# Kernel optimization log

Measured on AMD Instinct MI355X. Metric: run time of the kernel, lower is better.

The kernel has to match this reference:

```python
import jax, jax.numpy as jnp
import numpy as np

SR = 22050
HOP = 512
BINS_PER_OCTAVE = 24
N_OCTAVES = 7
N_BINS = BINS_PER_OCTAVE * N_OCTAVES  # 168
FMIN = 32.7  # center_bins with bins_per_semitone=1 leaves fmin unchanged


def _make_cqt_kernels():
    """Right-aligned (causal) complex CQT kernels, 24 bins/octave, 7 octaves.

    This is the explicit math the stateful SlidingCqt24 C++ routine computes
    incrementally: for each bin k with center freq f_k = fmin * 2^(k/24),
    a Hann-windowed complex exponential of length N_k = ceil(Q*sr/f_k),
    Q = 1/(2^(1/24)-1). Bins are ordered ascending in frequency, matching the
    per-octave np.flip layout of the original forward.
    """
    Q = 1.0 / (2.0 ** (1.0 / BINS_PER_OCTAVE) - 1.0)
    freqs = FMIN * 2.0 ** (np.arange(N_BINS) / BINS_PER_OCTAVE)
    lens = np.ceil(Q * SR / freqs).astype(np.int64)
    n_max = int(lens.max())  # 23014
    kr = np.zeros((N_BINS, n_max), dtype=np.float32)
    ki = np.zeros((N_BINS, n_max), dtype=np.float32)
    for k in range(N_BINS):  # small fixed loop over 168 bins (setup only)
        n = int(lens[k])
        t = np.arange(n)
        win = np.hanning(n)
        c = win * np.exp(2j * np.pi * freqs[k] * t / SR) / n
        kr[k, n_max - n:] = c.real.astype(np.float32)
        ki[k, n_max - n:] = c.imag.astype(np.float32)
    return kr, ki


def setup_inputs() -> dict:
    key = jax.random.key(0)
    audio = jax.random.normal(key, (4, 1, 352768), dtype=jnp.float32)
    kr, ki = _make_cqt_kernels()
    return {
        "audio_waveforms": audio,
        "kern_real": jnp.asarray(kr),
        "kern_imag": jnp.asarray(ki),
    }


def reference(audio_waveforms, kern_real, kern_imag):
    # audio: [B, C, S]; kernels: [K, Nmax]
    n_max = kern_real.shape[1]
    B, C, S = audio_waveforms.shape
    n_blocks = S // HOP  # 689
    # Causal sliding window: block i analyzes the n_max samples ending at
    # sample (i+1)*HOP (left zero-pad for early blocks), matching the
    # block-streaming behavior of the sliding CQT.
    pad = n_max - HOP
    x = jnp.pad(audio_waveforms, ((0, 0), (0, 0), (pad, 0)))
    # Strided frame gather: [n_blocks, Nmax] index table.
    idx = jnp.arange(n_blocks)[:, None] * HOP + jnp.arange(n_max)[None, :]
    frames = x[..., idx]  # [B, C, T, Nmax]
    re = jnp.einsum("bctn,kn->bctk", frames, kern_real)
    im = jnp.einsum("bctn,kn->bctk", frames, kern_imag)
    mag = jnp.sqrt(re * re + im * im)  # [B, C, n_blocks, n_bins]
    return mag
```

## Files before the change

kernel.cpp:

```cpp
#include <hip/hip_runtime.h>
#include <math.h>


namespace {
constexpr int kSR    = 22050;
constexpr int kHop   = 512;
constexpr int kBins  = 168;
constexpr int kT     = 689;
constexpr int kB     = 4;
constexpr int kS     = 352768;
constexpr float kKScale    = 4096.0f;
constexpr float kKScaleInv = 1.0f / 4096.0f;
constexpr int kG16 = 11;
constexpr int kAcc = kB * kT * kBins * 2;
constexpr int kTPadB   = 768;
constexpr int kBinPadB = 176;
constexpr int kAccB    = kB * kTPadB * kBinPadB * 2;
}

typedef _Float16 half8 __attribute__((ext_vector_type(8)));
typedef _Float16 half2v __attribute__((ext_vector_type(2)));
typedef float floatx4 __attribute__((ext_vector_type(4)));

struct Jobs {
  int k0[48];
  int lo[48];
  int hi[48];
  int n;
};

struct JobsC {
  int lo16[kG16];
  int cb16[kG16];
  int mlo[3];
  int sm[24];
  int slo[24];
  int shi[24];
  int ns;
  int totch;
};

__device__ inline void atomAddF(float* p, float v) {
  __hip_atomic_fetch_add(p, v, __ATOMIC_RELAXED, __HIP_MEMORY_SCOPE_AGENT);
}

typedef __attribute__((address_space(3))) unsigned int lds_uint;
typedef __attribute__((address_space(1))) const unsigned int glb_uint;
__device__ __forceinline__ void dma16(const void* g, void* l) {
  __builtin_amdgcn_global_load_lds((glb_uint*)g, (lds_uint*)l, 16, 0, 0);
}

__global__ __launch_bounds__(256) void prep_fused(
    const float* __restrict__ x, const float* __restrict__ kr,
    const float* __restrict__ ki, _Float16* __restrict__ xp,
    _Float16* __restrict__ bp, float* __restrict__ accb,
    const int pad, const int xps, const int nmax,
    const int nbx, const int nbp, const JobsC jt) {
  int bid = blockIdx.x;
  const int tid = threadIdx.x;

  if (bid < nbx) {
    const int octx = xps >> 3;
    const int gid = bid * 256 + tid;
    if (gid >= kB * octx) return;
    const int b = gid / octx;
    const int i = (gid - b * octx) * 8;
    const float* xb = x + (size_t)b * kS - pad;
    half8 h;
    #pragma unroll
    for (int j = 0; j < 8; ++j) {
      const int e = i + j;
      h[j] = (e >= pad && e < pad + kS) ? (_Float16)xb[e] : (_Float16)0.f;
    }
    *(half8*)&xp[(size_t)b * xps + i] = h;
    return;
  }
  bid -= nbx;

  if (bid < nbp) {
    const int chunkid = bid * 4 + (tid >> 6);
    const int lane = tid & 63;
    if (chunkid >= jt.totch) return;
    int g = 0;
    #pragma unroll
    for (int j = 1; j < kG16; ++j)
      if (chunkid >= jt.cb16[j]) g = j;
    const int c = chunkid - jt.cb16[g];
    const int mm = lane & 15;
    const int q  = lane >> 4;
    const int bin  = g * 16 + mm;
    const int col0 = jt.lo16[g] + c * 32 + q * 8;
    const bool binok = (bin < kBins);
    const float* rowr = kr + (size_t)bin * nmax;
    const float* rowi = ki + (size_t)bin * nmax;
    half8 hre, him;
    #pragma unroll
    for (int j = 0; j < 8; ++j) {
      const int col = col0 + j;
      const bool ok = binok && (col < nmax);
      hre[j] = ok ? (_Float16)(rowr[col] * kKScale) : (_Float16)0.f;
      him[j] = ok ? (_Float16)(rowi[col] * kKScale) : (_Float16)0.f;
    }
    _Float16* dst = bp + (size_t)chunkid * 1024 + lane * 8;
    *(half8*)dst = hre;
    *(half8*)(dst + 512) = him;
    return;
  }
  bid -= nbp;

  const int idx = (bid * 256 + tid) * 4;
  if (idx < kAcc)
    *(floatx4*)&accb[idx] = (floatx4){0.f, 0.f, 0.f, 0.f};
}

__global__ __launch_bounds__(256) void cqt_mfma9(
    const _Float16* __restrict__ bp, const _Float16* __restrict__ xp,
    float* __restrict__ accb, const int xps, const JobsC jt) {
  __shared__ _Float16 lds[2][10240];

  const int sx = blockIdx.y;
  const int fb = blockIdx.x >> 2;
  const int b  = blockIdx.x & 3;
  const int tid  = threadIdx.x;
  const int wave = tid >> 6;
  const int lane = tid & 63;
  const int mm = lane & 15;
  const int q  = lane >> 4;
  const int mac = jt.sm[sx];
  const int g16 = mac * 4 + wave;
  const bool gvalid = (g16 < kG16);
  const int mlo = jt.mlo[mac];
  const int gs = gvalid ? ((jt.lo16[g16] - mlo) >> 5) : 0x7fffffff;
  const int slo = jt.slo[sx];
  const int shi = jt.shi[sx];
  const int fbase = fb * 32;

  const _Float16* xb = xp + (size_t)b * xps;
  int aoff;
  {
    const int tl = wave & 1;
    int row = fbase + tl * 16 + mm;
    if (row > kT - 1) row = kT - 1;
    aoff = row * kHop + q * 8 + ((wave >> 1) * 32);
  }
  const _Float16* bgrp =
      gvalid ? (bp + (size_t)(jt.cb16[g16] - gs) * 1024 + lane * 8) : bp;

  floatx4 accr[2], acci[2];
  #pragma unroll
  for (int tl = 0; tl < 2; ++tl) {
    accr[tl] = (floatx4){0.f, 0.f, 0.f, 0.f};
    acci[tl] = (floatx4){0.f, 0.f, 0.f, 0.f};
  }

  auto stageDMA = [&](int c, int buf) {
    _Float16* L = lds[buf];
    dma16(xb + mlo + c * 32 + aoff, L + wave * 512);
    if (gvalid && c >= gs) {
      const _Float16* bs = bgrp + (size_t)c * 1024;
      #pragma unroll
      for (int cc = 0; cc < 2; ++cc)
        #pragma unroll
        for (int ri = 0; ri < 2; ++ri)
          dma16(bs + cc * 1024 + ri * 512,
                L + 2048 + (wave * 4 + cc * 2 + ri) * 512);
    }
  };

  auto compute = [&](int c, int buf) {
    if (!gvalid || c < gs) return;
    const _Float16* L = lds[buf];
    #pragma unroll
    for (int cc = 0; cc < 2; ++cc) {
      const half8 Bre = *(const half8*)(L + 2048 + (wave * 4 + cc * 2) * 512 + lane * 8);
      const half8 Bim = *(const half8*)(L + 2048 + (wave * 4 + cc * 2 + 1) * 512 + lane * 8);
      #pragma unroll
      for (int tl = 0; tl < 2; ++tl) {
        const half8 A = *(const half8*)(L + (cc * 2 + tl) * 512 + lane * 8);
        accr[tl] = __builtin_amdgcn_mfma_f32_16x16x32_f16(A, Bre, accr[tl], 0, 0, 0);
        acci[tl] = __builtin_amdgcn_mfma_f32_16x16x32_f16(A, Bim, acci[tl], 0, 0, 0);
      }
    }
  };

  stageDMA(slo, 0);
  int buf = 0;
  #pragma unroll 1
  for (int c = slo; c < shi; c += 2) {
    __syncthreads();
    if (c + 2 < shi) stageDMA(c + 2, buf ^ 1);
    compute(c, buf);
    buf ^= 1;
  }

  const int bin = g16 * 16 + mm;
  if (bin < kBins) {
    #pragma unroll
    for (int tl = 0; tl < 2; ++tl) {
      const int tb = fbase + tl * 16 + q * 4;
      #pragma unroll
      for (int r = 0; r < 4; ++r) {
        const int t = tb + r;
        if (t < kT) {
          const size_t o = (((size_t)b * kT + t) * kBins + bin) * 2;
          atomAddF(&accb[o],     accr[tl][r] * kKScaleInv);
          atomAddF(&accb[o + 1], acci[tl][r] * kKScaleInv);
        }
      }
    }
  }
}

__global__ __launch_bounds__(256) void cqt_mag4(
    const float* __restrict__ accb, float* __restrict__ out) {
  const int gid = (blockIdx.x * 256 + threadIdx.x) * 4;
  if (gid >= kB * kT * kBins) return;
  const floatx4 v0 = *(const floatx4*)&accb[gid * 2];
  const floatx4 v1 = *(const floatx4*)&accb[gid * 2 + 4];
  floatx4 o;
  o[0] = sqrtf(v0[0] * v0[0] + v0[1] * v0[1]);
  o[1] = sqrtf(v0[2] * v0[2] + v0[3] * v0[3]);
  o[2] = sqrtf(v1[0] * v1[0] + v1[1] * v1[1]);
  o[3] = sqrtf(v1[2] * v1[2] + v1[3] * v1[3]);
  *(floatx4*)&out[gid] = o;
}

__global__ __launch_bounds__(256) void cqt_mag_final(
    const float* __restrict__ accb, float* __restrict__ out,
    const int tp, const int kp) {
  int gid = blockIdx.x * 256 + threadIdx.x;
  if (gid >= kB * kT * kBins) return;
  const int k = gid % kBins;
  const int r = gid / kBins;
  const int t = r % kT;
  const int b = r / kT;
  const float2 v = ((const float2*)accb)[((size_t)b * tp + t) * kp + k];
  out[gid] = sqrtf(v.x * v.x + v.y * v.y);
}

__global__ __launch_bounds__(256) void prep_x_kernel(
    const float* __restrict__ x, _Float16* __restrict__ xp,
    const int pad, const int xps) {
  const int halfx = xps >> 1;
  int gid = blockIdx.x * 256 + threadIdx.x;
  if (gid >= kB * halfx) return;
  const int b = gid / halfx;
  const int i = (gid - b * halfx) * 2;
  float v0 = 0.f, v1 = 0.f;
  if (i     >= pad && i     < pad + kS) v0 = x[(size_t)b * kS + (i - pad)];
  if (i + 1 >= pad && i + 1 < pad + kS) v1 = x[(size_t)b * kS + (i + 1 - pad)];
  half2v h; h.x = (_Float16)v0; h.y = (_Float16)v1;
  *(half2v*)&xp[(size_t)b * xps + i] = h;
}

__global__ __launch_bounds__(256) void cqt_mfma_kernel(
    const float* __restrict__ kr, const float* __restrict__ ki,
    const _Float16* __restrict__ xp, float* __restrict__ accb,
    const int nmax, const int xps, const Jobs jt) {
  __shared__ _Float16 Bs[2][16][264];
  const int jb = blockIdx.x;
  const int k0   = jt.k0[jb];
  const int n_lo = jt.lo[jb];
  const int n_hi = jt.hi[jb];
  const int b  = blockIdx.z;
  const int fb = blockIdx.y;
  const int tid  = threadIdx.x;
  const int lane = tid & 63;
  const int wave = tid >> 6;
  const int m = lane & 15;
  const int q = lane >> 4;
  const int sbin = tid >> 4;
  const int scol = tid & 15;
  const int gbin = k0 + sbin;
  const bool binok = (gbin < kBins);
  const float* rowr = kr + (size_t)gbin * nmax;
  const float* rowi = ki + (size_t)gbin * nmax;
  const int fbase = fb * 256 + wave * 64;
  const _Float16* ax =
      xp + (size_t)b * xps + (size_t)(fbase + m) * kHop + q * 8;
  floatx4 accr[4], acci[4];
  #pragma unroll
  for (int tl = 0; tl < 4; ++tl) {
    accr[tl] = (floatx4){0.f, 0.f, 0.f, 0.f};
    acci[tl] = (floatx4){0.f, 0.f, 0.f, 0.f};
  }
  for (int n0r = n_lo; n0r < n_hi; n0r += 256) {
    __syncthreads();
    #pragma unroll
    for (int c = 0; c < 16; ++c) {
      const int col = n0r + scol + c * 16;
      const bool ok = binok && (col < nmax);
      const float vr = ok ? rowr[col] : 0.f;
      const float vi = ok ? rowi[col] : 0.f;
      Bs[0][sbin][scol + c * 16] = (_Float16)(vr * kKScale);
      Bs[1][sbin][scol + c * 16] = (_Float16)(vi * kKScale);
    }
    __syncthreads();
    const _Float16* axr = ax + n0r;
    #pragma unroll
    for (int c = 0; c < 8; ++c) {
      const int ko = c * 32 + q * 8;
      const half8 br = *(const half8*)&Bs[0][m][ko];
      const half8 bi = *(const half8*)&Bs[1][m][ko];
      #pragma unroll
      for (int tl = 0; tl < 4; ++tl) {
        const half8 a = *(const half8*)(axr + tl * 16 * kHop + c * 32);
        accr[tl] = __builtin_amdgcn_mfma_f32_16x16x32_f16(a, br, accr[tl], 0, 0, 0);
        acci[tl] = __builtin_amdgcn_mfma_f32_16x16x32_f16(a, bi, acci[tl], 0, 0, 0);
      }
    }
  }
  #pragma unroll
  for (int tl = 0; tl < 4; ++tl) {
    #pragma unroll
    for (int rr = 0; rr < 4; ++rr) {
      const int t = fbase + tl * 16 + q * 4 + rr;
      const size_t o = (((size_t)b * kTPadB + t) * kBinPadB + (k0 + m)) * 2;
      atomAddF(&accb[o],     accr[tl][rr] * kKScaleInv);
      atomAddF(&accb[o + 1], acci[tl][rr] * kKScaleInv);
    }
  }
}

namespace fb32 {
constexpr int TT = 8;
constexpr int KG = 4;
constexpr int kTTiles  = (kT + TT - 1) / TT;
constexpr int kKGroups = kBins / KG;
constexpr int kWaves   = kB * kTTiles * kKGroups;
}

__global__ __launch_bounds__(256) void cqt_mag_kernel(
    const float* __restrict__ x,
    const float* __restrict__ kr,
    const float* __restrict__ ki,
    float* __restrict__ out,
    const int nmax, const int pad) {
  using namespace fb32;
  const int wave = (blockIdx.x << 2) + (threadIdx.x >> 6);
  const int lane = threadIdx.x & 63;
  if (wave >= kWaves) return;
  const int kg    = wave / (kB * kTTiles);
  const int rem   = wave - kg * (kB * kTTiles);
  const int b     = rem / kTTiles;
  const int ttile = rem - b * kTTiles;
  const int k0 = kg * KG;
  const int t0 = ttile * TT;
  const double Q  = 1.0 / (exp2(1.0 / 24.0) - 1.0);
  const double f0 = 32.7 * exp2((double)k0 / 24.0);
  int N = (int)ceil(Q * (double)kSR / f0) + 8;
  int full_start = nmax - N;
  if (full_start < 0) full_start = 0;
  int tbase[TT], lo[TT], t_last;
  { int t = t0 + TT - 1; if (t > kT - 1) t = kT - 1; t_last = t; }
  #pragma unroll
  for (int tt = 0; tt < TT; ++tt) {
    int t = t0 + tt; if (t > kT - 1) t = kT - 1;
    tbase[tt] = b * kS + t * kHop - pad;
    lo[tt]    = pad - t * kHop;
  }
  int head_start = pad - t_last * kHop;
  if (head_start < full_start) head_start = full_start;
  int safe = pad - t0 * kHop;
  if (safe < head_start) safe = head_start;
  int body_start = nmax - ((nmax - safe) & ~63);
  float accr[TT][KG], acci[TT][KG];
  #pragma unroll
  for (int tt = 0; tt < TT; ++tt)
    #pragma unroll
    for (int kk = 0; kk < KG; ++kk) { accr[tt][kk] = 0.f; acci[tt][kk] = 0.f; }
  for (int n = body_start - 64; n > head_start - 64; n -= 64) {
    const int nn = n + lane;
    const bool kok = (nn >= 0);
    float krv[KG], kiv[KG];
    #pragma unroll
    for (int kk = 0; kk < KG; ++kk) {
      krv[kk] = kok ? kr[(k0 + kk) * nmax + nn] : 0.f;
      kiv[kk] = kok ? ki[(k0 + kk) * nmax + nn] : 0.f;
    }
    float a[TT];
    #pragma unroll
    for (int tt = 0; tt < TT; ++tt)
      a[tt] = (nn >= lo[tt]) ? x[tbase[tt] + nn] : 0.f;
    #pragma unroll
    for (int tt = 0; tt < TT; ++tt)
      #pragma unroll
      for (int kk = 0; kk < KG; ++kk) {
        accr[tt][kk] = fmaf(a[tt], krv[kk], accr[tt][kk]);
        acci[tt][kk] = fmaf(a[tt], kiv[kk], acci[tt][kk]);
      }
  }
  for (int n = body_start; n < nmax; n += 64) {
    const int nn = n + lane;
    float krv[KG], kiv[KG];
    #pragma unroll
    for (int kk = 0; kk < KG; ++kk) {
      krv[kk] = kr[(k0 + kk) * nmax + nn];
      kiv[kk] = ki[(k0 + kk) * nmax + nn];
    }
    float a[TT];
    #pragma unroll
    for (int tt = 0; tt < TT; ++tt)
      a[tt] = x[tbase[tt] + nn];
    #pragma unroll
    for (int tt = 0; tt < TT; ++tt)
      #pragma unroll
      for (int kk = 0; kk < KG; ++kk) {
        accr[tt][kk] = fmaf(a[tt], krv[kk], accr[tt][kk]);
        acci[tt][kk] = fmaf(a[tt], kiv[kk], acci[tt][kk]);
      }
  }
  #pragma unroll
  for (int tt = 0; tt < TT; ++tt) {
    #pragma unroll
    for (int kk = 0; kk < KG; ++kk) {
      float r = accr[tt][kk];
      float i = acci[tt][kk];
      #pragma unroll
      for (int s = 32; s > 0; s >>= 1) {
        r += __shfl_xor(r, s, 64);
        i += __shfl_xor(i, s, 64);
      }
      if (lane == 0) {
        const int t = t0 + tt;
        if (t < kT)
          out[(b * kT + t) * kBins + (k0 + kk)] = sqrtf(r * r + i * i);
      }
    }
  }
}

extern "C" void kernel_launch(void* const* d_in, const int* in_sizes, int n_in,
                              void* d_out, int out_size, void* d_ws, size_t ws_size,
                              hipStream_t stream) {
  const float* x  = (const float*)d_in[0];
  const float* kr = (const float*)d_in[1];
  const float* ki = (const float*)d_in[2];
  float* out = (float*)d_out;

  const int nmax = in_sizes[1] / kBins;
  const int pad  = nmax - kHop;

  const int kcap = ((nmax + 255) / 256) * 256;
  const double Q = 1.0 / (exp2(1.0 / 24.0) - 1.0);

  JobsC jc;
  int tot = 0;
  for (int g = 0; g < kG16; ++g) {
    const double f0 = 32.7 * exp2((double)(16 * g) / 24.0);
    const int N = (int)ceil(Q * (double)kSR / f0) + 8;
    int lo = nmax - N;
    if (lo < 0) lo = 0;
    lo &= ~255;
    jc.lo16[g] = lo;
    jc.cb16[g] = tot;
    tot += (kcap - lo) / 32;
  }
  jc.totch = tot;
  int ns = 0;
  for (int m = 0; m < 3; ++m) {
    jc.mlo[m] = jc.lo16[4 * m];
    const int C = (kcap - jc.mlo[m]) / 32;
    const int nsl = (C + 95) / 96;
    const int len = ((C + nsl - 1) / nsl + 1) & ~1;
    for (int s = 0; s < nsl && ns < 24; ++s) {
      const int lo = s * len;
      if (lo >= C) break;
      int hi = lo + len;
      if (hi > C) hi = C;
      jc.sm[ns] = m; jc.slo[ns] = lo; jc.shi[ns] = hi;
      ++ns;
    }
  }
  jc.ns = ns;

  const int xpsA = (kT - 1) * kHop + kcap + 256;
  const size_t xpA_bytes = (size_t)kB * xpsA * sizeof(_Float16);
  const size_t accA_off  = (xpA_bytes + 511) & ~(size_t)511;
  const size_t accA_bytes = (size_t)kAcc * sizeof(float);
  const size_t bpA_off   = (accA_off + accA_bytes + 511) & ~(size_t)511;
  const size_t bpA_bytes = (size_t)tot * 2048;
  const size_t ws_A = bpA_off + bpA_bytes;

  const int xpsB = (kTPadB - 1) * kHop + kcap + 256;
  const size_t xpB_bytes = (size_t)kB * xpsB * sizeof(_Float16);
  const size_t accB_off  = (xpB_bytes + 511) & ~(size_t)511;
  const size_t accB_bytes = (size_t)kAccB * sizeof(float);
  const size_t ws_B = accB_off + accB_bytes;

  if (ws_size >= ws_A) {
    _Float16* xp = (_Float16*)d_ws;
    float* accb  = (float*)((char*)d_ws + accA_off);
    _Float16* bp = (_Float16*)((char*)d_ws + bpA_off);

    const int nbx = (kB * (xpsA / 8) + 255) / 256;
    const int nbp = (tot + 3) / 4;
    const int nba = (kAcc / 4 + 255) / 256;
    prep_fused<<<nbx + nbp + nba, 256, 0, stream>>>(
        x, kr, ki, xp, bp, accb, pad, xpsA, nmax, nbx, nbp, jc);

    {
      dim3 grid(88, ns);
      cqt_mfma9<<<grid, 256, 0, stream>>>(bp, xp, accb, xpsA, jc);
    }
    {
      const int total = kB * kT * kBins;
      cqt_mag4<<<(total / 4 + 255) / 256, 256, 0, stream>>>(accb, out);
    }
    return;
  }

  if (ws_size >= ws_B) {
    _Float16* xp = (_Float16*)d_ws;
    float* accb  = (float*)((char*)d_ws + accB_off);
    Jobs jt;
    int nj = 0;
    for (int g = 0; g < 11; ++g) {
      const int gk0 = 16 * g;
      const double f0 = 32.7 * exp2((double)gk0 / 24.0);
      const int N = (int)ceil(Q * (double)kSR / f0) + 8;
      int lo = nmax - N;
      if (lo < 0) lo = 0;
      lo = (lo / 2048) * 2048;
      for (int s = lo; s < kcap && nj < 48; s += 2048) {
        jt.k0[nj] = gk0;
        jt.lo[nj] = s;
        jt.hi[nj] = (s + 2048 < kcap) ? s + 2048 : kcap;
        ++nj;
      }
    }
    jt.n = nj;
    hipMemsetAsync(accb, 0, accB_bytes, stream);
    {
      const int total = kB * (xpsB / 2);
      prep_x_kernel<<<(total + 255) / 256, 256, 0, stream>>>(x, xp, pad, xpsB);
    }
    {
      dim3 grid(nj, kTPadB / 256, kB);
      cqt_mfma_kernel<<<grid, 256, 0, stream>>>(kr, ki, xp, accb, nmax, xpsB, jt);
    }
    {
      const int total = kB * kT * kBins;
      cqt_mag_final<<<(total + 255) / 256, 256, 0, stream>>>(
          accb, out, kTPadB, kBinPadB);
    }
    return;
  }

  {
    const int blocks = fb32::kWaves / 4;
    cqt_mag_kernel<<<blocks, 256, 0, stream>>>(x, kr, ki, out, nmax, pad);
  }
}
```

Measured before the change: 128.4 us.

## Replace atomic split-K accumulation with fp16 partial buffers and reduce in magnitude pass

```diff
diff --git a/kernel.cpp b/kernel.cpp
--- a/kernel.cpp
+++ b/kernel.cpp
@@ -12,6 +12,7 @@
 constexpr float kKScale    = 4096.0f;
 constexpr float kKScaleInv = 1.0f / 4096.0f;
 constexpr int kG16 = 11;
+constexpr int kFBB = 88;
 constexpr int kAcc = kB * kT * kBins * 2;
 constexpr int kTPadB   = 768;
 constexpr int kBinPadB = 176;
@@ -36,6 +37,8 @@
   int sm[24];
   int slo[24];
   int shi[24];
+  int sbeg[3];
+  int scnt[3];
   int ns;
   int totch;
 };
@@ -113,9 +116,11 @@
     *(floatx4*)&accb[idx] = (floatx4){0.f, 0.f, 0.f, 0.f};
 }
 
-__global__ __launch_bounds__(256) void cqt_mfma9(
+template <bool PARTIAL>
+__global__ __launch_bounds__(256) void cqt_mfma_t(
     const _Float16* __restrict__ bp, const _Float16* __restrict__ xp,
-    float* __restrict__ accb, const int xps, const JobsC jt) {
+    float* __restrict__ accb, _Float16* __restrict__ part,
+    const int xps, const JobsC jt) {
   __shared__ _Float16 lds[2][10240];
 
   const int sx = blockIdx.y;
@@ -193,19 +198,83 @@
     buf ^= 1;
   }
 
-  const int bin = g16 * 16 + mm;
-  if (bin < kBins) {
-    #pragma unroll
-    for (int tl = 0; tl < 2; ++tl) {
-      const int tb = fbase + tl * 16 + q * 4;
+  if (PARTIAL) {
+    _Float16* pw = part +
+        (((size_t)sx * kFBB + blockIdx.x) * 4 + wave) * 1024 + lane * 16;
+    half8 p0, p1;
+    #pragma unroll
+    for (int r = 0; r < 4; ++r) {
+      p0[r * 2]     = (_Float16)accr[0][r];
+      p0[r * 2 + 1] = (_Float16)acci[0][r];
+      p1[r * 2]     = (_Float16)accr[1][r];
+      p1[r * 2 + 1] = (_Float16)acci[1][r];
+    }
+    *(half8*)pw = p0;
+    *(half8*)(pw + 8) = p1;
+  } else {
+    const int bin = g16 * 16 + mm;
+    if (bin < kBins) {
       #pragma unroll
-      for (int r = 0; r < 4; ++r) {
-        const int t = tb + r;
-        if (t < kT) {
-          const size_t o = (((size_t)b * kT + t) * kBins + bin) * 2;
-          atomAddF(&accb[o],     accr[tl][r] * kKScaleInv);
-          atomAddF(&accb[o + 1], acci[tl][r] * kKScaleInv);
+      for (int tl = 0; tl < 2; ++tl) {
+        const int tb = fbase + tl * 16 + q * 4;
+        #pragma unroll
+        for (int r = 0; r < 4; ++r) {
+          const int t = tb + r;
+          if (t < kT) {
+            const size_t o = (((size_t)b * kT + t) * kBins + bin) * 2;
+            atomAddF(&accb[o],     accr[tl][r] * kKScaleInv);
+            atomAddF(&accb[o + 1], acci[tl][r] * kKScaleInv);
+          }
         }
+      }
+    }
+  }
+}
+
+__global__ __launch_bounds__(256) void cqt_mag_part(
+    const _Float16* __restrict__ part, float* __restrict__ out,
+    const JobsC jt) {
+  const int fbb = blockIdx.x;
+  const int fb = fbb >> 2;
+  const int b  = fbb & 3;
+  const int wave = threadIdx.x >> 6;
+  const int lane = threadIdx.x & 63;
+  const int g16 = blockIdx.y * 4 + wave;
+  if (g16 >= kG16) return;
+  const int mac = g16 >> 2;
+  const int w   = g16 & 3;
+  const int mm = lane & 15;
+  const int q  = lane >> 4;
+
+  float a[16];
+  #pragma unroll
+  for (int i = 0; i < 16; ++i) a[i] = 0.f;
+  const int s0 = jt.sbeg[mac];
+  const int s1 = s0 + jt.scnt[mac];
+  #pragma unroll 1
+  for (int s = s0; s < s1; ++s) {
+    const _Float16* p = part +
+        (((size_t)s * kFBB + fbb) * 4 + w) * 1024 + lane * 16;
+    const half8 v0 = *(const half8*)p;
+    const half8 v1 = *(const half8*)(p + 8);
+    #pragma unroll
+    for (int j = 0; j < 8; ++j) {
+      a[j]     += (float)v0[j];
+      a[8 + j] += (float)v1[j];
+    }
+  }
+  const int k = g16 * 16 + mm;
+  if (k >= kBins) return;
+  #pragma unroll
+  for (int tl = 0; tl < 2; ++tl) {
+    #pragma unroll
+    for (int r = 0; r < 4; ++r) {
+      const int t = fb * 32 + tl * 16 + q * 4 + r;
+      if (t < kT) {
+        const float re = a[tl * 8 + r * 2];
+        const float im = a[tl * 8 + r * 2 + 1];
+        out[((size_t)b * kT + t) * kBins + k] =
+            sqrtf(re * re + im * im) * kKScaleInv;
       }
     }
   }
@@ -460,6 +529,7 @@
   int ns = 0;
   for (int m = 0; m < 3; ++m) {
     jc.mlo[m] = jc.lo16[4 * m];
+    jc.sbeg[m] = ns;
     const int C = (kcap - jc.mlo[m]) / 32;
     const int nsl = (C + 95) / 96;
     const int len = ((C + nsl - 1) / nsl + 1) & ~1;
@@ -471,15 +541,22 @@
       jc.sm[ns] = m; jc.slo[ns] = lo; jc.shi[ns] = hi;
       ++ns;
     }
+    jc.scnt[m] = ns - jc.sbeg[m];
   }
   jc.ns = ns;
 
   const int xpsA = (kT - 1) * kHop + kcap + 256;
   const size_t xpA_bytes = (size_t)kB * xpsA * sizeof(_Float16);
+  const size_t bpA_bytes = (size_t)tot * 2048;
+
+  const size_t partP_off   = (xpA_bytes + 511) & ~(size_t)511;
+  const size_t partP_bytes = (size_t)ns * kFBB * 4 * 1024 * sizeof(_Float16);
+  const size_t bpP_off     = (partP_off + partP_bytes + 511) & ~(size_t)511;
+  const size_t ws_P = bpP_off + bpA_bytes;
+
   const size_t accA_off  = (xpA_bytes + 511) & ~(size_t)511;
   const size_t accA_bytes = (size_t)kAcc * sizeof(float);
   const size_t bpA_off   = (accA_off + accA_bytes + 511) & ~(size_t)511;
-  const size_t bpA_bytes = (size_t)tot * 2048;
   const size_t ws_A = bpA_off + bpA_bytes;
 
   const int xpsB = (kTPadB - 1) * kHop + kcap + 256;
@@ -488,20 +565,41 @@
   const size_t accB_bytes = (size_t)kAccB * sizeof(float);
   const size_t ws_B = accB_off + accB_bytes;
 
+  const int nbx = (kB * (xpsA / 8) + 255) / 256;
+  const int nbp = (tot + 3) / 4;
+
+  if (ws_size >= ws_P) {
+    _Float16* xp   = (_Float16*)d_ws;
+    _Float16* part = (_Float16*)((char*)d_ws + partP_off);
+    _Float16* bp   = (_Float16*)((char*)d_ws + bpP_off);
+
+    prep_fused<<<nbx + nbp, 256, 0, stream>>>(
+        x, kr, ki, xp, bp, (float*)part , pad, xpsA, nmax,
+        nbx, nbp, jc);
+    {
+      dim3 grid(kFBB, ns);
+      cqt_mfma_t<true><<<grid, 256, 0, stream>>>(
+          bp, xp, nullptr, part, xpsA, jc);
+    }
+    {
+      dim3 grid(kFBB, 3);
+      cqt_mag_part<<<grid, 256, 0, stream>>>(part, out, jc);
+    }
+    return;
+  }
+
   if (ws_size >= ws_A) {
     _Float16* xp = (_Float16*)d_ws;
     float* accb  = (float*)((char*)d_ws + accA_off);
     _Float16* bp = (_Float16*)((char*)d_ws + bpA_off);
 
-    const int nbx = (kB * (xpsA / 8) + 255) / 256;
-    const int nbp = (tot + 3) / 4;
     const int nba = (kAcc / 4 + 255) / 256;
     prep_fused<<<nbx + nbp + nba, 256, 0, stream>>>(
         x, kr, ki, xp, bp, accb, pad, xpsA, nmax, nbx, nbp, jc);
-
     {
-      dim3 grid(88, ns);
-      cqt_mfma9<<<grid, 256, 0, stream>>>(bp, xp, accb, xpsA, jc);
+      dim3 grid(kFBB, ns);
+      cqt_mfma_t<false><<<grid, 256, 0, stream>>>(
+          bp, xp, accb, nullptr, xpsA, jc);
     }
     {
       const int total = kB * kT * kBins;
```

Result: faster. 121.7 us (-5.2%).
